# Kernel tuning notes

Measured on AMD Instinct MI355X. Metric: run time of the kernel, lower is better.

The kernel has to match this reference:

```python
import jax, jax.numpy as jnp
import numpy as np

N = 50000      # nodes
E = 800000     # edges (before self-loops)
G = 64         # graphs
F_IN = 128     # n_attr
OUT = 128      # size_vect
NEG_SLOPE = 0.2


def setup_inputs() -> dict:
    key = jax.random.key(0)
    ks = jax.random.split(key, 48)
    def rn(i, shape, s=0.05):
        return (jax.random.normal(ks[i], shape, jnp.float32) * s)
    x = jax.random.normal(ks[0], (N, F_IN), jnp.float32)
    src = jax.random.randint(ks[1], (E,), 0, N, jnp.int32)
    dst = jax.random.randint(ks[2], (E,), 0, N, jnp.int32)
    dst = jnp.where(dst == src, (dst + 1) % N, dst)  # no pre-existing self-loops
    edge_index = jnp.stack([src, dst])
    batch = jnp.sort(jax.random.randint(ks[3], (N,), 0, G, jnp.int32))
    inp = {"x": x, "edge_index": edge_index, "batch": batch}
    # GATConv params (heads=1): W [in,out], att_src/att_dst [out], bias [out]
    dims = [(F_IN, 64), (64, 128), (128, 256)]
    for li, (di, do) in enumerate(dims, start=1):
        b = 4 + (li - 1) * 4
        inp[f"W{li}"] = rn(b, (di, do))
        inp[f"asrc{li}"] = rn(b + 1, (do,))
        inp[f"adst{li}"] = rn(b + 2, (do,))
        inp[f"b{li}"] = rn(b + 3, (do,))
    # dense tail: Linear stored as [in,out]
    dense = {"d1": (512, 256), "d2": (256, 128), "d3": (128, 64),
             "mean": (256, 64), "d4": (64, 64), "d5": (64, 128),
             "d6": (128, 256), "d7": (256, OUT)}
    i = 20
    for name, (di, do) in dense.items():
        inp[f"{name}_w"] = rn(i, (di, do))
        inp[f"{name}_b"] = rn(i + 1, (do,))
        i += 2
    return inp


def _gat_conv(x, src, dst, W, a_src, a_dst, b):
    h = x @ W                                   # [N, out]
    e = (h @ a_src)[src] + (h @ a_dst)[dst]     # [E']
    e = jnp.where(e > 0, e, NEG_SLOPE * e)      # LeakyReLU(0.2)
    m = jax.ops.segment_max(e, dst, num_segments=N)
    ex = jnp.exp(e - m[dst])
    denom = jax.ops.segment_sum(ex, dst, num_segments=N)
    alpha = ex / denom[dst]                     # segment softmax over incoming edges
    out = jax.ops.segment_sum(h[src] * alpha[:, None], dst, num_segments=N)
    return out + b


def reference(x, edge_index, batch,
              W1, asrc1, adst1, b1, W2, asrc2, adst2, b2, W3, asrc3, adst3, b3,
              d1_w, d1_b, d2_w, d2_b, d3_w, d3_b, mean_w, mean_b,
              d4_w, d4_b, d5_w, d5_b, d6_w, d6_b, d7_w, d7_b):
    ar = jnp.arange(N, dtype=edge_index.dtype)
    src = jnp.concatenate([edge_index[0], ar])  # add self-loops (PyG default)
    dst = jnp.concatenate([edge_index[1], ar])
    h = _gat_conv(x, src, dst, W1, asrc1, adst1, b1)
    h = _gat_conv(h, src, dst, W2, asrc2, adst2, b2)
    h = _gat_conv(h, src, dst, W3, asrc3, adst3, b3)   # [N, 256]
    x1 = jax.ops.segment_max(h, batch, num_segments=G)
    x2 = jax.ops.segment_sum(h, batch, num_segments=G)
    cnt = jax.ops.segment_sum(jnp.ones((N,), h.dtype), batch, num_segments=G)
    x3 = x2 / jnp.maximum(cnt, 1.0)[:, None]
    z = jnp.concatenate([x1, x2], axis=-1)              # [G, 512]
    z = jax.nn.relu(z @ d1_w + d1_b)
    z = jax.nn.relu(z @ d2_w + d2_b)
    z = jax.nn.relu(z @ d3_w + d3_b)
    z = z * jax.nn.sigmoid(x3 @ mean_w + mean_b)
    z = jax.nn.relu(z @ d4_w + d4_b)                    # dropout = identity (eval)
    z = jax.nn.relu(z @ d5_w + d5_b)
    z = jax.nn.relu(z @ d6_w + d6_b)
    return z @ d7_w + d7_b
```

## Files before the change

kernel.cpp:

```cpp
#include <hip/hip_runtime.h>
#include <hip/hip_bf16.h>
#include <math.h>

#define NN 50000
#define NE 800000
#define NEP 850000
#define NG 64
#define CAP 64

#define NBKT 49
#define BMAX 20480
#define EPB  3125
#define KE   13

typedef unsigned short u16;
typedef __attribute__((ext_vector_type(8))) short short8;
typedef __attribute__((ext_vector_type(4))) float f32x4;

__device__ __forceinline__ float bfu2f(u16 u) {
    return __uint_as_float((unsigned)u << 16);
}
__device__ __forceinline__ u16 f2bfu(float f) {
    __hip_bfloat16 h = __float2bfloat16(f);
    union { __hip_bfloat16 h; u16 u; } c; c.h = h; return c.u;
}

__device__ __forceinline__ unsigned fkey(float f) {
    unsigned u = __float_as_uint(f);
    return (u & 0x80000000u) ? ~u : (u | 0x80000000u);
}
__device__ __forceinline__ float fkey_inv(unsigned k) {
    return (k & 0x80000000u) ? __uint_as_float(k ^ 0x80000000u) : __uint_as_float(~k);
}

__global__ void k_init(int* __restrict__ deg, u16* __restrict__ srcsort,
                       int* __restrict__ poolbuf, int IB,
                       const float* __restrict__ W0, const float* __restrict__ as0, const float* __restrict__ ad0,
                       u16* __restrict__ Wb0, float* __restrict__ wa0, float* __restrict__ wb0,
                       const float* __restrict__ W1, const float* __restrict__ as1, const float* __restrict__ ad1,
                       u16* __restrict__ Wb1, float* __restrict__ wa1, float* __restrict__ wb1,
                       const float* __restrict__ W2, const float* __restrict__ as2, const float* __restrict__ ad2,
                       u16* __restrict__ Wb2, float* __restrict__ wa2, float* __restrict__ wb2) {
    __shared__ float pas[4], pbs[4];
    int tid = threadIdx.x;
    if (blockIdx.x < IB) {
        int i = blockIdx.x * 256 + tid;
        if (i < NN) {
            deg[i] = 1;
            srcsort[i << 6] = (u16)i;
        } else if (i - NN < NG * 512 + NG + 64) {
            poolbuf[i - NN] = 0;
        }
        return;
    }
    int b = blockIdx.x - IB;
    const float *W, *asv, *adv; u16* Wb; float *wa, *wb; int k, dout;
    if (b < 128)      { W = W0; asv = as0; adv = ad0; Wb = Wb0; wa = wa0; wb = wb0; k = b;       dout = 64;  }
    else if (b < 192) { W = W1; asv = as1; adv = ad1; Wb = Wb1; wa = wa1; wb = wb1; k = b - 128; dout = 128; }
    else              { W = W2; asv = as2; adv = ad2; Wb = Wb2; wa = wa2; wb = wb2; k = b - 192; dout = 256; }
    float pa = 0.f, pb = 0.f;
    for (int n = tid; n < dout; n += 256) {
        float w = W[(size_t)k * dout + n];
        Wb[(size_t)k * dout + n] = f2bfu(w);
        pa += w * asv[n];
        pb += w * adv[n];
    }
#pragma unroll
    for (int off = 32; off; off >>= 1) {
        pa += __shfl_xor(pa, off);
        pb += __shfl_xor(pb, off);
    }
    if ((tid & 63) == 0) { pas[tid >> 6] = pa; pbs[tid >> 6] = pb; }
    __syncthreads();
    if (tid == 0) {
        wa[k] = pas[0] + pas[1] + pas[2] + pas[3];
        wb[k] = pbs[0] + pbs[1] + pbs[2] + pbs[3];
    }
}

__global__ __launch_bounds__(256) void k_bin(const int* __restrict__ src, const int* __restrict__ dst,
                                             unsigned* __restrict__ ebuf, int* __restrict__ bcur) {
    __shared__ int hist[NBKT], gbase[NBKT];
    int tid = threadIdx.x;
    int e0 = blockIdx.x * EPB;
    if (tid < NBKT) hist[tid] = 0;
    __syncthreads();
    unsigned pk[KE];
    unsigned br[KE];
#pragma unroll
    for (int k = 0; k < KE; k++) {
        int e = tid + k * 256;
        pk[k] = 0; br[k] = 0xffffffffu;
        if (e < EPB) {
            int sv = src[e0 + e];
            int dv = dst[e0 + e];
            int bkt = dv >> 10;
            int r = atomicAdd(&hist[bkt], 1);
            pk[k] = (unsigned)sv | ((unsigned)(dv & 1023) << 16);
            br[k] = ((unsigned)bkt << 16) | (unsigned)r;
        }
    }
    __syncthreads();
    if (tid < NBKT) gbase[tid] = atomicAdd(&bcur[tid], hist[tid]);
    __syncthreads();
#pragma unroll
    for (int k = 0; k < KE; k++) {
        if (br[k] != 0xffffffffu) {
            int bkt = (int)(br[k] >> 16);
            int r   = (int)(br[k] & 0xffffu);
            ebuf[(size_t)bkt * BMAX + gbase[bkt] + r] = pk[k];
        }
    }
}

template<int DIN, int DOUT, bool XF32, bool STIN, bool STOUT>
__device__ __forceinline__ void gemm_body(int bx, const void* __restrict__ Xin,
                                          const u16* __restrict__ Wb,
                                          u16* __restrict__ Hb,
                                          const float* __restrict__ bias,
                                          const float* __restrict__ wav,
                                          const float* __restrict__ wbv,
                                          float* __restrict__ sout,
                                          float* __restrict__ tout) {
    constexpr int KS = DIN / 32;
    constexpr int CT = DOUT / 16;
    constexpr int TPW = CT / 4;
    constexpr int STRIDE = DIN + 16;
    constexpr int SRN = STOUT ? 256 : 1;
    __shared__ u16 Xs[64 * STRIDE];
    __shared__ float sred[SRN], tred[SRN];
    int tid = threadIdx.x, wave = tid >> 6, lane = tid & 63;
    int quad = lane >> 4, l15 = lane & 15;
    int n0 = bx * 64;

    short8 bfr[TPW][KS];
#pragma unroll
    for (int ct = 0; ct < TPW; ct++) {
        int nb = (wave * TPW + ct) * 16 + l15;
#pragma unroll
        for (int ks = 0; ks < KS; ks++) {
            int kb = ks * 32 + quad * 8;
            short8 b;
#pragma unroll
            for (int j = 0; j < 8; j++) b[j] = (short)Wb[(size_t)(kb + j) * DOUT + nb];
            bfr[ct][ks] = b;
        }
    }

    for (int c = tid; c < 64 * DIN / 8; c += 256) {
        int row = (c * 8) / DIN, col = (c * 8) % DIN;
        int rg = n0 + row; if (rg >= NN) rg = NN - 1;
        u16 v[8];
        if constexpr (XF32) {
            const float* p = (const float*)Xin + (size_t)rg * DIN + col;
            float4 f0 = *(const float4*)p;
            float4 f1 = *(const float4*)(p + 4);
            v[0] = f2bfu(f0.x); v[1] = f2bfu(f0.y); v[2] = f2bfu(f0.z); v[3] = f2bfu(f0.w);
            v[4] = f2bfu(f1.x); v[5] = f2bfu(f1.y); v[6] = f2bfu(f1.z); v[7] = f2bfu(f1.w);
            if constexpr (STIN) {
                float pa = f0.x * wav[col]     + f0.y * wav[col + 1]
                         + f0.z * wav[col + 2] + f0.w * wav[col + 3]
                         + f1.x * wav[col + 4] + f1.y * wav[col + 5]
                         + f1.z * wav[col + 6] + f1.w * wav[col + 7];
                float pb = f0.x * wbv[col]     + f0.y * wbv[col + 1]
                         + f0.z * wbv[col + 2] + f0.w * wbv[col + 3]
                         + f1.x * wbv[col + 4] + f1.y * wbv[col + 5]
                         + f1.z * wbv[col + 6] + f1.w * wbv[col + 7];
                constexpr int RT = DIN / 8;
#pragma unroll
                for (int off = RT / 2; off; off >>= 1) {
                    pa += __shfl_xor(pa, off);
                    pb += __shfl_xor(pb, off);
                }
                if ((tid & (RT - 1)) == 0 && (n0 + row) < NN) {
                    sout[n0 + row] = pa;
                    tout[n0 + row] = pb;
                }
            }
        } else {
            const u16* p = (const u16*)Xin + (size_t)rg * DIN + col;
            ushort4 a = *(const ushort4*)p;
            ushort4 b = *(const ushort4*)(p + 4);
            v[0] = a.x; v[1] = a.y; v[2] = a.z; v[3] = a.w;
            v[4] = b.x; v[5] = b.y; v[6] = b.z; v[7] = b.w;
        }
        u16* d = &Xs[row * STRIDE + col];
#pragma unroll
        for (int j = 0; j < 8; j++) d[j] = v[j];
    }
    __syncthreads();

#pragma unroll
    for (int rt = 0; rt < 4; rt++) {
        short8 afr[KS];
#pragma unroll
        for (int ks = 0; ks < KS; ks++)
            afr[ks] = *(const short8*)&Xs[(rt * 16 + l15) * STRIDE + ks * 32 + quad * 8];
        float sp[4] = {0.f, 0.f, 0.f, 0.f};
        float tp[4] = {0.f, 0.f, 0.f, 0.f};
#pragma unroll
        for (int ct = 0; ct < TPW; ct++) {
            f32x4 cf = {0.f, 0.f, 0.f, 0.f};
#pragma unroll
            for (int ks = 0; ks < KS; ks++)
                cf = __builtin_amdgcn_mfma_f32_16x16x32_bf16(afr[ks], bfr[ct][ks], cf, 0, 0, 0);
            int col = (wave * TPW + ct) * 16 + l15;
            float bv = bias ? bias[col] : 0.f;
            int rbase = n0 + rt * 16 + quad * 4;
#pragma unroll
            for (int reg = 0; reg < 4; reg++) {
                int r = rbase + reg;
                float v = cf[reg] + bv;
                if (r < NN) Hb[(size_t)r * DOUT + col] = f2bfu(v);
                if constexpr (STOUT) {
                    sp[reg] += v * wav[col];
                    tp[reg] += v * wbv[col];
                }
            }
        }
        if constexpr (STOUT) {
#pragma unroll
            for (int reg = 0; reg < 4; reg++) {
                float a = sp[reg], b = tp[reg];
#pragma unroll
                for (int off = 8; off; off >>= 1) {
                    a += __shfl_xor(a, off);
                    b += __shfl_xor(b, off);
                }
                if (l15 == 0) {
                    int idx = wave * 64 + rt * 16 + quad * 4 + reg;
                    sred[idx] = a;
                    tred[idx] = b;
                }
            }
        }
    }
    if constexpr (STOUT) {
        __syncthreads();
        if (tid < 64 && (n0 + tid) < NN) {
            sout[n0 + tid] = sred[tid] + sred[64 + tid] + sred[128 + tid] + sred[192 + tid];
            tout[n0 + tid] = tred[tid] + tred[64 + tid] + tred[128 + tid] + tred[192 + tid];
        }
    }
}

__global__ __launch_bounds__(256) void k_front(const unsigned* __restrict__ ebuf,
                                               const int* __restrict__ bcur,
                                               int* __restrict__ deg, u16* __restrict__ srcsort,
                                               const float* __restrict__ x_in,
                                               const u16* __restrict__ Wb0, u16* __restrict__ Hb,
                                               const float* __restrict__ wa, const float* __restrict__ wb,
                                               float* __restrict__ s, float* __restrict__ t) {
    int tid = threadIdx.x;
    if (blockIdx.x < NBKT) {
        __shared__ int cnt[1024];
        int bkt = blockIdx.x;
        int base = bkt << 10;
        for (int i = tid; i < 1024; i += 256) cnt[i] = 1;
        __syncthreads();
        int n = bcur[bkt];
        const unsigned* eb = ebuf + (size_t)bkt * BMAX;
        for (int e = tid; e < n; e += 256) {
            unsigned p = eb[e];
            int sv = (int)(p & 0xffffu);
            int dl = (int)(p >> 16);
            int pos = atomicAdd(&cnt[dl], 1);
            if (pos < CAP) srcsort[((base + dl) << 6) + pos] = (u16)sv;
        }
        __syncthreads();
        for (int i = tid; i < 1024; i += 256) {
            int node = base + i;
            if (node < NN) deg[node] = cnt[i];
        }
        return;
    }
    gemm_body<128, 64, true, true, false>(blockIdx.x - NBKT, x_in, Wb0, Hb, nullptr, wa, wb, s, t);
}

template<int DIN, int DOUT>
__global__ __launch_bounds__(256) void k_gemm_b(const u16* __restrict__ Xin,
                                                const u16* __restrict__ Wb,
                                                u16* __restrict__ Hb,
                                                const float* __restrict__ bias) {
    gemm_body<DIN, DOUT, false, false, false>(blockIdx.x, Xin, Wb, Hb, bias,
                                              nullptr, nullptr, nullptr, nullptr);
}

template<int DIN, int DOUT>
__global__ __launch_bounds__(256) void k_gemm_st(const u16* __restrict__ Xin,
                                                 const u16* __restrict__ Wb,
                                                 u16* __restrict__ Hb,
                                                 const float* __restrict__ bias,
                                                 const float* __restrict__ wav,
                                                 const float* __restrict__ wbv,
                                                 float* __restrict__ s,
                                                 float* __restrict__ t) {
    gemm_body<DIN, DOUT, false, false, true>(blockIdx.x, Xin, Wb, Hb, bias, wav, wbv, s, t);
}

__global__ void k_agg1(const int* __restrict__ deg, const u16* __restrict__ srcsort,
                       const float* __restrict__ s, const float* __restrict__ t,
                       const u16* __restrict__ Hb, const float* __restrict__ bias,
                       u16* __restrict__ OUT, const float* __restrict__ wan,
                       const float* __restrict__ wbn, float* __restrict__ sout,
                       float* __restrict__ tout) {
    constexpr int GS = 8;
    constexpr int P  = 8;
    int node = blockIdx.x * 4 + (threadIdx.x >> 6);
    int lane = threadIdx.x & 63;
    if (node >= NN) return;
    int cnt = min(deg[node], CAP);
    float tn = t[node];
    int sv = 0; float ex = 0.f;
    if (lane < cnt) {
        sv = srcsort[(node << 6) + lane];
        float e = s[sv] + tn;
        e = (e > 0.f) ? e : 0.2f * e;
        ex = expf(e);
    }
    float dsum = ex;
#pragma unroll
    for (int off = 32; off; off >>= 1) dsum += __shfl_xor(dsum, off);
    ex *= 1.f / dsum;

    int sg = lane / GS;
    int pg = lane % GS;
    float acc[8];
#pragma unroll
    for (int e = 0; e < 8; e++) acc[e] = 0.f;

    for (int q = 0; q < cnt; q += P) {
        int myq = q + sg;
        int mq = (myq < cnt) ? myq : q;
        float a = __shfl(ex, mq);
        int  idx = __shfl(sv, mq);
        if (myq >= cnt) a = 0.f;
        uint4 u = *(const uint4*)(Hb + (size_t)idx * 64 + pg * 8);
        acc[0] += a * bfu2f((u16)(u.x & 0xffff));
        acc[1] += a * bfu2f((u16)(u.x >> 16));
        acc[2] += a * bfu2f((u16)(u.y & 0xffff));
        acc[3] += a * bfu2f((u16)(u.y >> 16));
        acc[4] += a * bfu2f((u16)(u.z & 0xffff));
        acc[5] += a * bfu2f((u16)(u.z >> 16));
        acc[6] += a * bfu2f((u16)(u.w & 0xffff));
        acc[7] += a * bfu2f((u16)(u.w >> 16));
    }

#pragma unroll
    for (int step = GS; step < 64; step <<= 1) {
#pragma unroll
        for (int e = 0; e < 8; e++) acc[e] += __shfl_xor(acc[e], step);
    }
#pragma unroll
    for (int e = 0; e < 8; e++) acc[e] += bias[pg * 8 + e];

    {
        float pa = 0.f, pb = 0.f;
#pragma unroll
        for (int e = 0; e < 8; e++) {
            pa += acc[e] * wan[pg * 8 + e];
            pb += acc[e] * wbn[pg * 8 + e];
        }
#pragma unroll
        for (int off = 32; off; off >>= 1) {
            pa += __shfl_xor(pa, off);
            pb += __shfl_xor(pb, off);
        }
        if (lane == 0) { sout[node] = pa * (1.f / P); tout[node] = pb * (1.f / P); }
    }

    if (sg == 0) {
        uint4 o;
        o.x = (unsigned)f2bfu(acc[0]) | ((unsigned)f2bfu(acc[1]) << 16);
        o.y = (unsigned)f2bfu(acc[2]) | ((unsigned)f2bfu(acc[3]) << 16);
        o.z = (unsigned)f2bfu(acc[4]) | ((unsigned)f2bfu(acc[5]) << 16);
        o.w = (unsigned)f2bfu(acc[6]) | ((unsigned)f2bfu(acc[7]) << 16);
        *(uint4*)(OUT + (size_t)node * 64 + pg * 8) = o;
    }
}

template<int DIN>
__global__ void k_aggX(const int* __restrict__ deg, const u16* __restrict__ srcsort,
                       const float* __restrict__ s, const float* __restrict__ t,
                       const u16* __restrict__ X, u16* __restrict__ OUT) {
    constexpr int GS = DIN / 8;
    constexpr int P  = 64 / GS;
    int node = blockIdx.x * 4 + (threadIdx.x >> 6);
    int lane = threadIdx.x & 63;
    if (node >= NN) return;
    int cnt = min(deg[node], CAP);
    float tn = t[node];
    int sv = 0; float ex = 0.f;
    if (lane < cnt) {
        sv = srcsort[(node << 6) + lane];
        float e = s[sv] + tn;
        e = (e > 0.f) ? e : 0.2f * e;
        ex = expf(e);
    }
    float dsum = ex;
#pragma unroll
    for (int off = 32; off; off >>= 1) dsum += __shfl_xor(dsum, off);
    ex *= 1.f / dsum;

    int sg = lane / GS;
    int pg = lane % GS;
    float acc[8];
#pragma unroll
    for (int e = 0; e < 8; e++) acc[e] = 0.f;

    for (int q = 0; q < cnt; q += P) {
        int myq = q + sg;
        int mq = (myq < cnt) ? myq : q;
        float a = __shfl(ex, mq);
        int  idx = __shfl(sv, mq);
        if (myq >= cnt) a = 0.f;
        uint4 u = *(const uint4*)(X + (size_t)idx * DIN + pg * 8);
        acc[0] += a * bfu2f((u16)(u.x & 0xffff));
        acc[1] += a * bfu2f((u16)(u.x >> 16));
        acc[2] += a * bfu2f((u16)(u.y & 0xffff));
        acc[3] += a * bfu2f((u16)(u.y >> 16));
        acc[4] += a * bfu2f((u16)(u.z & 0xffff));
        acc[5] += a * bfu2f((u16)(u.z >> 16));
        acc[6] += a * bfu2f((u16)(u.w & 0xffff));
        acc[7] += a * bfu2f((u16)(u.w >> 16));
    }

#pragma unroll
    for (int step = GS; step < 64; step <<= 1) {
#pragma unroll
        for (int e = 0; e < 8; e++) acc[e] += __shfl_xor(acc[e], step);
    }

    if (sg == 0) {
        uint4 o;
        o.x = (unsigned)f2bfu(acc[0]) | ((unsigned)f2bfu(acc[1]) << 16);
        o.y = (unsigned)f2bfu(acc[2]) | ((unsigned)f2bfu(acc[3]) << 16);
        o.z = (unsigned)f2bfu(acc[4]) | ((unsigned)f2bfu(acc[5]) << 16);
        o.w = (unsigned)f2bfu(acc[6]) | ((unsigned)f2bfu(acc[7]) << 16);
        *(uint4*)(OUT + (size_t)node * DIN + pg * 8) = o;
    }
}

__global__ void k_pool2(const u16* __restrict__ H, const int* __restrict__ batch,
                        unsigned* __restrict__ x1k, float* __restrict__ x2,
                        float* __restrict__ cnt) {
    int c0 = blockIdx.x * 64;
    if (c0 >= NN) return;
    int o = threadIdx.x;
    int endn = min(c0 + 64, NN);
    int g = batch[c0];
    float mx = -INFINITY, sm = 0.f, cl = 0.f;
    for (int nd = c0; nd < endn; nd++) {
        int bg = batch[nd];
        if (bg != g) {
            atomicMax(&x1k[g * 256 + o], fkey(mx));
            atomicAdd(&x2[g * 256 + o], sm);
            if (o == 0) atomicAdd(&cnt[g], cl);
            g = bg; mx = -INFINITY; sm = 0.f; cl = 0.f;
        }
        float hv = bfu2f(H[(size_t)nd * 256 + o]);
        mx = fmaxf(mx, hv);
        sm += hv;
        cl += 1.f;
    }
    atomicMax(&x1k[g * 256 + o], fkey(mx));
    atomicAdd(&x2[g * 256 + o], sm);
    if (o == 0) atomicAdd(&cnt[g], cl);
}

template<int DIN, int DOUT, int ACT>
__device__ __forceinline__ void dense_layer(const float* __restrict__ in,
                                            const float* __restrict__ W,
                                            const float* __restrict__ B,
                                            float* __restrict__ out, int o,
                                            float* __restrict__ red) {
    constexpr int T = 1024 / DOUT;
    constexpr int KS = DIN / T;
    int oo = o % DOUT;
    int kk = o / DOUT;
    int kbase = kk * KS;
    float p0 = 0.f, p1 = 0.f, p2 = 0.f, p3 = 0.f;
#pragma unroll 4
    for (int k = 0; k < KS; k += 4) {
        p0 += in[kbase + k]     * W[(size_t)(kbase + k) * DOUT + oo];
        p1 += in[kbase + k + 1] * W[(size_t)(kbase + k + 1) * DOUT + oo];
        p2 += in[kbase + k + 2] * W[(size_t)(kbase + k + 2) * DOUT + oo];
        p3 += in[kbase + k + 3] * W[(size_t)(kbase + k + 3) * DOUT + oo];
    }
    float p = (p0 + p1) + (p2 + p3);
    red[o] = p;
    __syncthreads();
    if (o < DOUT) {
#pragma unroll
        for (int tt = 1; tt < T; tt++) p += red[oo + tt * DOUT];
        p += B[oo];
        if constexpr (ACT == 1) p = fmaxf(p, 0.f);
        else if constexpr (ACT == 2) p = 1.f / (1.f + expf(-p));
        out[oo] = p;
    }
    __syncthreads();
}

__global__ __launch_bounds__(1024) void k_tail(const unsigned* __restrict__ x1k, const float* __restrict__ x2,
                       const float* __restrict__ cnt,
                       const float* __restrict__ d1w, const float* __restrict__ d1b,
                       const float* __restrict__ d2w, const float* __restrict__ d2b,
                       const float* __restrict__ d3w, const float* __restrict__ d3b,
                       const float* __restrict__ mw,  const float* __restrict__ mb,
                       const float* __restrict__ d4w, const float* __restrict__ d4b,
                       const float* __restrict__ d5w, const float* __restrict__ d5b,
                       const float* __restrict__ d6w, const float* __restrict__ d6b,
                       const float* __restrict__ d7w, const float* __restrict__ d7b,
                       float* __restrict__ out) {
    __shared__ float z[512];
    __shared__ float A[256];
    __shared__ float Bf[256];
    __shared__ float red[1024];
    __shared__ float x3s[256];
    __shared__ float gbuf[64];
    int g = blockIdx.x, o = threadIdx.x;
    if (o < 256) {
        float c = fmaxf(cnt[g], 1.f);
        float sv = x2[(size_t)g * 256 + o];
        z[o] = fkey_inv(x1k[(size_t)g * 256 + o]);
        z[256 + o] = sv;
        x3s[o] = sv / c;
    }
    __syncthreads();
    dense_layer<512, 256, 1>(z,   d1w, d1b, A,    o, red);
    dense_layer<256, 128, 1>(A,   d2w, d2b, Bf,   o, red);
    dense_layer<128,  64, 1>(Bf,  d3w, d3b, A,    o, red);
    dense_layer<256,  64, 2>(x3s, mw,  mb,  gbuf, o, red);
    if (o < 64) A[o] *= gbuf[o];
    __syncthreads();
    dense_layer< 64,  64, 1>(A,   d4w, d4b, Bf,   o, red);
    dense_layer< 64, 128, 1>(Bf,  d5w, d5b, A,    o, red);
    dense_layer<128, 256, 1>(A,   d6w, d6b, z,    o, red);
    dense_layer<256, 128, 0>(z,   d7w, d7b, A,    o, red);
    if (o < 128) out[(size_t)g * 128 + o] = A[o];
}

extern "C" void kernel_launch(void* const* d_in, const int* in_sizes, int n_in,
                              void* d_out, int out_size, void* d_ws, size_t ws_size,
                              hipStream_t stream) {
    const float* x_in  = (const float*)d_in[0];
    const int*   ei    = (const int*)d_in[1];
    const int*   batch = (const int*)d_in[2];
    const int* src = ei;
    const int* dst = ei + NE;

    const float* Wl[3]  = { (const float*)d_in[3], (const float*)d_in[7],  (const float*)d_in[11] };
    const float* asl[3] = { (const float*)d_in[4], (const float*)d_in[8],  (const float*)d_in[12] };
    const float* adl[3] = { (const float*)d_in[5], (const float*)d_in[9],  (const float*)d_in[13] };
    const float* bl[3]  = { (const float*)d_in[6], (const float*)d_in[10], (const float*)d_in[14] };

    const float* d1w = (const float*)d_in[15]; const float* d1b = (const float*)d_in[16];
    const float* d2w = (const float*)d_in[17]; const float* d2b = (const float*)d_in[18];
    const float* d3w = (const float*)d_in[19]; const float* d3b = (const float*)d_in[20];
    const float* mw  = (const float*)d_in[21]; const float* mb  = (const float*)d_in[22];
    const float* d4w = (const float*)d_in[23]; const float* d4b = (const float*)d_in[24];
    const float* d5w = (const float*)d_in[25]; const float* d5b = (const float*)d_in[26];
    const float* d6w = (const float*)d_in[27]; const float* d6b = (const float*)d_in[28];
    const float* d7w = (const float*)d_in[29]; const float* d7b = (const float*)d_in[30];

    float* ws = (float*)d_ws;
    size_t off = 0;
    u16* Hb1 = (u16*)(ws + off); off += (size_t)NN * 32;
    u16* Xb1 = (u16*)(ws + off); off += (size_t)NN * 32;
    u16* A2  = (u16*)(ws + off); off += (size_t)NN * 32;
    u16* H2  = (u16*)(ws + off); off += (size_t)NN * 64;
    u16* A3  = (u16*)(ws + off); off += (size_t)NN * 64;
    u16* Xb3 = (u16*)(ws + off); off += (size_t)NN * 128;
    float* sA = ws + off; off += NN;
    float* tA = ws + off; off += NN;
    float* sB = ws + off; off += NN;
    float* tB = ws + off; off += NN;
    u16* Wb0 = (u16*)(ws + off); off += (128 * 64) / 2;
    u16* Wb1 = (u16*)(ws + off); off += (64 * 128) / 2;
    u16* Wb2 = (u16*)(ws + off); off += (128 * 256) / 2;
    float* wa0 = ws + off; off += 128;  float* wb0 = ws + off; off += 128;
    float* wa1 = ws + off; off += 64;   float* wb1 = ws + off; off += 64;
    float* wa2 = ws + off; off += 128;  float* wb2 = ws + off; off += 128;
    unsigned* x1k = (unsigned*)(ws + off); off += NG * 256;
    float* x2    = ws + off; off += NG * 256;
    float* cnt   = ws + off; off += NG;
    int* bcur    = (int*)(ws + off); off += 64;
    int* ip      = (int*)(ws + off);
    int* deg     = ip;               ip += NN;
    u16* srcsort = (u16*)ip;         ip += (NN * CAP) / 2;
    unsigned* ebuf = (unsigned*)Xb3;

    const int GB = (NN + 63) / 64;
    const int AB = (NN + 3) / 4;
    const int IB = (NN + NG * 512 + NG + 64 + 255) / 256;

    k_init<<<IB + 320, 256, 0, stream>>>(deg, srcsort, (int*)x1k, IB,
                                         Wl[0], asl[0], adl[0], Wb0, wa0, wb0,
                                         Wl[1], asl[1], adl[1], Wb1, wa1, wb1,
                                         Wl[2], asl[2], adl[2], Wb2, wa2, wb2);
    k_bin<<<256, 256, 0, stream>>>(src, dst, ebuf, bcur);
    k_front<<<NBKT + GB, 256, 0, stream>>>(ebuf, bcur, deg, srcsort,
                                           x_in, Wb0, Hb1, wa0, wb0, sA, tA);

    k_agg1<<<AB, 256, 0, stream>>>(deg, srcsort, sA, tA, Hb1, bl[0], Xb1, wa1, wb1, sB, tB);

    k_aggX<64><<<AB, 256, 0, stream>>>(deg, srcsort, sB, tB, Xb1, A2);
    k_gemm_st<64, 128><<<GB, 256, 0, stream>>>(A2, Wb1, H2, bl[1], wa2, wb2, sA, tA);

    k_aggX<128><<<AB, 256, 0, stream>>>(deg, srcsort, sA, tA, H2, A3);
    k_gemm_b<128, 256><<<GB, 256, 0, stream>>>(A3, Wb2, Xb3, bl[2]);

    k_pool2<<<(NN + 63) / 64, 256, 0, stream>>>(Xb3, batch, x1k, x2, cnt);
    k_tail<<<NG, 1024, 0, stream>>>(x1k, x2, cnt,
                                    d1w, d1b, d2w, d2b, d3w, d3b, mw, mb,
                                    d4w, d4b, d5w, d5b, d6w, d6b, d7w, d7b,
                                    (float*)d_out);
}
```

Measured before the change: 343.9 us.

## Fold layer-2 and layer-3 weights into one combined matrix and aggregate at 64 wide

Precomputes Wc = W2·W3 and the folded bias b2·W3 + b3 in the init kernel. Layer 3's attention scores then come from the 64-wide aggregate A2 plus a constant term. Because aggregation is linear, layer-3 aggregation now runs on 64-wide features instead of 128-wide, and the separate 64→128 GEMM plus its score-reduction epilogue are dropped. A single 64→256 GEMM remains. This removes one kernel launch and halves the gather width of the last aggregation, at the cost of extra bf16 rounding from the folded weights and a small extra matmul in init.

```diff
diff --git a/kernel.cpp b/kernel.cpp
--- a/kernel.cpp
+++ b/kernel.cpp
@@ -40,7 +40,10 @@
                        const float* __restrict__ W1, const float* __restrict__ as1, const float* __restrict__ ad1,
                        u16* __restrict__ Wb1, float* __restrict__ wa1, float* __restrict__ wb1,
                        const float* __restrict__ W2, const float* __restrict__ as2, const float* __restrict__ ad2,
-                       u16* __restrict__ Wb2, float* __restrict__ wa2, float* __restrict__ wb2) {
+                       const float* __restrict__ b2f, const float* __restrict__ b3f,
+                       u16* __restrict__ Wcb, float* __restrict__ bcv,
+                       float* __restrict__ wa2c, float* __restrict__ wb2c,
+                       float* __restrict__ cst) {
     __shared__ float pas[4], pbs[4];
     int tid = threadIdx.x;
     if (blockIdx.x < IB) {
@@ -54,27 +57,72 @@
         return;
     }
     int b = blockIdx.x - IB;
-    const float *W, *asv, *adv; u16* Wb; float *wa, *wb; int k, dout;
-    if (b < 128)      { W = W0; asv = as0; adv = ad0; Wb = Wb0; wa = wa0; wb = wb0; k = b;       dout = 64;  }
-    else if (b < 192) { W = W1; asv = as1; adv = ad1; Wb = Wb1; wa = wa1; wb = wb1; k = b - 128; dout = 128; }
-    else              { W = W2; asv = as2; adv = ad2; Wb = Wb2; wa = wa2; wb = wb2; k = b - 192; dout = 256; }
-    float pa = 0.f, pb = 0.f;
-    for (int n = tid; n < dout; n += 256) {
-        float w = W[(size_t)k * dout + n];
-        Wb[(size_t)k * dout + n] = f2bfu(w);
-        pa += w * asv[n];
-        pb += w * adv[n];
-    }
-#pragma unroll
-    for (int off = 32; off; off >>= 1) {
-        pa += __shfl_xor(pa, off);
-        pb += __shfl_xor(pb, off);
-    }
-    if ((tid & 63) == 0) { pas[tid >> 6] = pa; pbs[tid >> 6] = pb; }
-    __syncthreads();
-    if (tid == 0) {
-        wa[k] = pas[0] + pas[1] + pas[2] + pas[3];
-        wb[k] = pbs[0] + pbs[1] + pbs[2] + pbs[3];
+    if (b < 192) {
+        const float *W, *asv, *adv; u16* Wb; float *wa, *wb; int k, dout;
+        if (b < 128) { W = W0; asv = as0; adv = ad0; Wb = Wb0; wa = wa0; wb = wb0; k = b;       dout = 64;  }
+        else         { W = W1; asv = as1; adv = ad1; Wb = Wb1; wa = wa1; wb = wb1; k = b - 128; dout = 128; }
+        float pa = 0.f, pb = 0.f;
+        for (int n = tid; n < dout; n += 256) {
+            float w = W[(size_t)k * dout + n];
+            Wb[(size_t)k * dout + n] = f2bfu(w);
+            pa += w * asv[n];
+            pb += w * adv[n];
+        }
+#pragma unroll
+        for (int off = 32; off; off >>= 1) {
+            pa += __shfl_xor(pa, off);
+            pb += __shfl_xor(pb, off);
+        }
+        if ((tid & 63) == 0) { pas[tid >> 6] = pa; pbs[tid >> 6] = pb; }
+        __syncthreads();
+        if (tid == 0) {
+            wa[k] = pas[0] + pas[1] + pas[2] + pas[3];
+            wb[k] = pbs[0] + pbs[1] + pbs[2] + pbs[3];
+        }
+        return;
+    }
+    if (b < 256) {
+        int k = b - 192;
+        int o = tid;
+        float wc = 0.f;
+        const float* wrow = W1 + (size_t)k * 128;
+#pragma unroll 4
+        for (int j = 0; j < 128; j++) wc += wrow[j] * W2[(size_t)j * 256 + o];
+        Wcb[(size_t)k * 256 + o] = f2bfu(wc);
+        float pa = wc * as2[o];
+        float pb = wc * ad2[o];
+#pragma unroll
+        for (int off = 32; off; off >>= 1) {
+            pa += __shfl_xor(pa, off);
+            pb += __shfl_xor(pb, off);
+        }
+        if ((tid & 63) == 0) { pas[tid >> 6] = pa; pbs[tid >> 6] = pb; }
+        __syncthreads();
+        if (tid == 0) {
+            wa2c[k] = pas[0] + pas[1] + pas[2] + pas[3];
+            wb2c[k] = pbs[0] + pbs[1] + pbs[2] + pbs[3];
+        }
+        return;
+    }
+    {
+        int o = tid;
+        float t = 0.f;
+#pragma unroll 4
+        for (int j = 0; j < 128; j++) t += b2f[j] * W2[(size_t)j * 256 + o];
+        bcv[o] = t + b3f[o];
+        float ps = t * as2[o];
+        float pt = t * ad2[o];
+#pragma unroll
+        for (int off = 32; off; off >>= 1) {
+            ps += __shfl_xor(ps, off);
+            pt += __shfl_xor(pt, off);
+        }
+        if ((tid & 63) == 0) { pas[tid >> 6] = ps; pbs[tid >> 6] = pt; }
+        __syncthreads();
+        if (tid == 0) {
+            cst[0] = pas[0] + pas[1] + pas[2] + pas[3];
+            cst[1] = pbs[0] + pbs[1] + pbs[2] + pbs[3];
+        }
     }
 }
 
@@ -113,7 +161,7 @@
     }
 }
 
-template<int DIN, int DOUT, bool XF32, bool STIN, bool STOUT>
+template<int DIN, int DOUT, bool XF32, bool STIN>
 __device__ __forceinline__ void gemm_body(int bx, const void* __restrict__ Xin,
                                           const u16* __restrict__ Wb,
                                           u16* __restrict__ Hb,
@@ -126,9 +174,7 @@
     constexpr int CT = DOUT / 16;
     constexpr int TPW = CT / 4;
     constexpr int STRIDE = DIN + 16;
-    constexpr int SRN = STOUT ? 256 : 1;
     __shared__ u16 Xs[64 * STRIDE];
-    __shared__ float sred[SRN], tred[SRN];
     int tid = threadIdx.x, wave = tid >> 6, lane = tid & 63;
     int quad = lane >> 4, l15 = lane & 15;
     int n0 = bx * 64;
@@ -196,8 +242,6 @@
 #pragma unroll
         for (int ks = 0; ks < KS; ks++)
             afr[ks] = *(const short8*)&Xs[(rt * 16 + l15) * STRIDE + ks * 32 + quad * 8];
-        float sp[4] = {0.f, 0.f, 0.f, 0.f};
-        float tp[4] = {0.f, 0.f, 0.f, 0.f};
 #pragma unroll
         for (int ct = 0; ct < TPW; ct++) {
             f32x4 cf = {0.f, 0.f, 0.f, 0.f};
@@ -210,36 +254,8 @@
 #pragma unroll
             for (int reg = 0; reg < 4; reg++) {
                 int r = rbase + reg;
-                float v = cf[reg] + bv;
-                if (r < NN) Hb[(size_t)r * DOUT + col] = f2bfu(v);
-                if constexpr (STOUT) {
-                    sp[reg] += v * wav[col];
-                    tp[reg] += v * wbv[col];
-                }
+                if (r < NN) Hb[(size_t)r * DOUT + col] = f2bfu(cf[reg] + bv);
             }
-        }
-        if constexpr (STOUT) {
-#pragma unroll
-            for (int reg = 0; reg < 4; reg++) {
-                float a = sp[reg], b = tp[reg];
-#pragma unroll
-                for (int off = 8; off; off >>= 1) {
-                    a += __shfl_xor(a, off);
-                    b += __shfl_xor(b, off);
-                }
-                if (l15 == 0) {
-                    int idx = wave * 64 + rt * 16 + quad * 4 + reg;
-                    sred[idx] = a;
-                    tred[idx] = b;
-                }
-            }
-        }
-    }
-    if constexpr (STOUT) {
-        __syncthreads();
-        if (tid < 64 && (n0 + tid) < NN) {
-            sout[n0 + tid] = sred[tid] + sred[64 + tid] + sred[128 + tid] + sred[192 + tid];
-            tout[n0 + tid] = tred[tid] + tred[64 + tid] + tred[128 + tid] + tred[192 + tid];
         }
     }
 }
@@ -274,7 +290,7 @@
         }
         return;
     }
-    gemm_body<128, 64, true, true, false>(blockIdx.x - NBKT, x_in, Wb0, Hb, nullptr, wa, wb, s, t);
+    gemm_body<128, 64, true, true>(blockIdx.x - NBKT, x_in, Wb0, Hb, nullptr, wa, wb, s, t);
 }
 
 template<int DIN, int DOUT>
@@ -282,28 +298,17 @@
                                                 const u16* __restrict__ Wb,
                                                 u16* __restrict__ Hb,
                                                 const float* __restrict__ bias) {
-    gemm_body<DIN, DOUT, false, false, false>(blockIdx.x, Xin, Wb, Hb, bias,
-                                              nullptr, nullptr, nullptr, nullptr);
-}
-
-template<int DIN, int DOUT>
-__global__ __launch_bounds__(256) void k_gemm_st(const u16* __restrict__ Xin,
-                                                 const u16* __restrict__ Wb,
-                                                 u16* __restrict__ Hb,
-                                                 const float* __restrict__ bias,
-                                                 const float* __restrict__ wav,
-                                                 const float* __restrict__ wbv,
-                                                 float* __restrict__ s,
-                                                 float* __restrict__ t) {
-    gemm_body<DIN, DOUT, false, false, true>(blockIdx.x, Xin, Wb, Hb, bias, wav, wbv, s, t);
-}
-
+    gemm_body<DIN, DOUT, false, false>(blockIdx.x, Xin, Wb, Hb, bias,
+                                       nullptr, nullptr, nullptr, nullptr);
+}
+
+template<bool BIAS>
 __global__ void k_agg1(const int* __restrict__ deg, const u16* __restrict__ srcsort,
                        const float* __restrict__ s, const float* __restrict__ t,
                        const u16* __restrict__ Hb, const float* __restrict__ bias,
                        u16* __restrict__ OUT, const float* __restrict__ wan,
-                       const float* __restrict__ wbn, float* __restrict__ sout,
-                       float* __restrict__ tout) {
+                       const float* __restrict__ wbn, const float* __restrict__ cst,
+                       float* __restrict__ sout, float* __restrict__ tout) {
     constexpr int GS = 8;
     constexpr int P  = 8;
     int node = blockIdx.x * 4 + (threadIdx.x >> 6);
@@ -351,8 +356,10 @@
 #pragma unroll
         for (int e = 0; e < 8; e++) acc[e] += __shfl_xor(acc[e], step);
     }
-#pragma unroll
-    for (int e = 0; e < 8; e++) acc[e] += bias[pg * 8 + e];
+    if constexpr (BIAS) {
+#pragma unroll
+        for (int e = 0; e < 8; e++) acc[e] += bias[pg * 8 + e];
+    }
 
     {
         float pa = 0.f, pb = 0.f;
@@ -366,7 +373,12 @@
             pa += __shfl_xor(pa, off);
             pb += __shfl_xor(pb, off);
         }
-        if (lane == 0) { sout[node] = pa * (1.f / P); tout[node] = pb * (1.f / P); }
+        if (lane == 0) {
+            float cs = 0.f, ct_ = 0.f;
+            if constexpr (!BIAS) { cs = cst[0]; ct_ = cst[1]; }
+            sout[node] = pa * (1.f / P) + cs;
+            tout[node] = pb * (1.f / P) + ct_;
+        }
     }
 
     if (sg == 0) {
@@ -568,8 +580,9 @@
     u16* Hb1 = (u16*)(ws + off); off += (size_t)NN * 32;
     u16* Xb1 = (u16*)(ws + off); off += (size_t)NN * 32;
     u16* A2  = (u16*)(ws + off); off += (size_t)NN * 32;
-    u16* H2  = (u16*)(ws + off); off += (size_t)NN * 64;
-    u16* A3  = (u16*)(ws + off); off += (size_t)NN * 64;
+    u16* B3  = (u16*)(ws + off); off += (size_t)NN * 64;
+    float* bcv = ws + off; off += 256;
+    float* cst = ws + off; off += 64;
     u16* Xb3 = (u16*)(ws + off); off += (size_t)NN * 128;
     float* sA = ws + off; off += NN;
     float* tA = ws + off; off += NN;
@@ -577,10 +590,10 @@
     float* tB = ws + off; off += NN;
     u16* Wb0 = (u16*)(ws + off); off += (128 * 64) / 2;
     u16* Wb1 = (u16*)(ws + off); off += (64 * 128) / 2;
-    u16* Wb2 = (u16*)(ws + off); off += (128 * 256) / 2;
+    u16* Wcb = (u16*)(ws + off); off += (64 * 256) / 2;
     float* wa0 = ws + off; off += 128;  float* wb0 = ws + off; off += 128;
     float* wa1 = ws + off; off += 64;   float* wb1 = ws + off; off += 64;
-    float* wa2 = ws + off; off += 128;  float* wb2 = ws + off; off += 128;
+    float* wa2c = ws + off; off += 64;  float* wb2c = ws + off; off += 64;
     unsigned* x1k = (unsigned*)(ws + off); off += NG * 256;
     float* x2    = ws + off; off += NG * 256;
     float* cnt   = ws + off; off += NG;
@@ -594,21 +607,23 @@
     const int AB = (NN + 3) / 4;
     const int IB = (NN + NG * 512 + NG + 64 + 255) / 256;
 
-    k_init<<<IB + 320, 256, 0, stream>>>(deg, srcsort, (int*)x1k, IB,
+    k_init<<<IB + 257, 256, 0, stream>>>(deg, srcsort, (int*)x1k, IB,
                                          Wl[0], asl[0], adl[0], Wb0, wa0, wb0,
                                          Wl[1], asl[1], adl[1], Wb1, wa1, wb1,
-                                         Wl[2], asl[2], adl[2], Wb2, wa2, wb2);
+                                         Wl[2], asl[2], adl[2], bl[1], bl[2],
+                                         Wcb, bcv, wa2c, wb2c, cst);
     k_bin<<<256, 256, 0, stream>>>(src, dst, ebuf, bcur);
     k_front<<<NBKT + GB, 256, 0, stream>>>(ebuf, bcur, deg, srcsort,
                                            x_in, Wb0, Hb1, wa0, wb0, sA, tA);
 
-    k_agg1<<<AB, 256, 0, stream>>>(deg, srcsort, sA, tA, Hb1, bl[0], Xb1, wa1, wb1, sB, tB);
-
-    k_aggX<64><<<AB, 256, 0, stream>>>(deg, srcsort, sB, tB, Xb1, A2);
-    k_gemm_st<64, 128><<<GB, 256, 0, stream>>>(A2, Wb1, H2, bl[1], wa2, wb2, sA, tA);
-
-    k_aggX<128><<<AB, 256, 0, stream>>>(deg, srcsort, sA, tA, H2, A3);
-    k_gemm_b<128, 256><<<GB, 256, 0, stream>>>(A3, Wb2, Xb3, bl[2]);
+    k_agg1<true><<<AB, 256, 0, stream>>>(deg, srcsort, sA, tA, Hb1, bl[0],
+                                         Xb1, wa1, wb1, nullptr, sB, tB);
+
+    k_agg1<false><<<AB, 256, 0, stream>>>(deg, srcsort, sB, tB, Xb1, nullptr,
+                                          A2, wa2c, wb2c, cst, sA, tA);
+
+    k_aggX<64><<<AB, 256, 0, stream>>>(deg, srcsort, sA, tA, A2, B3);
+    k_gemm_b<64, 256><<<GB, 256, 0, stream>>>(B3, Wcb, Xb3, bcv);
 
     k_pool2<<<(NN + 63) / 64, 256, 0, stream>>>(Xb3, batch, x1k, x2, cnt);
     k_tail<<<NG, 1024, 0, stream>>>(x1k, x2, cnt,
```

Result: faster. 321.2 us (-6.6%).
